# Kernel tuning notes

Hardware: AMD Instinct MI355X
Metric: run time of the kernel (lower is better)

Reference implementation:

```python
import jax, jax.numpy as jnp
import numpy as np

HALF = 1          # half_size
KS = 2 * HALF + 1 # kernel size = 3
ALPHA = 0.05
ITER = 10
LOG_N = float(np.log(KS * KS))
EPS = 1e-8


def _dilate(x):
    # x: [B, 1, H, W] -- soft (log-sum-exp-like) dilation with entropy correction.
    B, C, H, W = x.shape
    xp = jnp.pad(x, ((0, 0), (0, 0), (HALF, HALF), (HALF, HALF)), mode='reflect')
    # Extract ks*ks shifted views -> patches [B, K, H, W] (C == 1 folded away);
    # ordering (ki, kj) matches torch.nn.Unfold's channel-major layout for C=1.
    patches = jnp.stack(
        [xp[:, 0, i:i + H, j:j + W] for i in range(KS) for j in range(KS)],
        axis=1,
    )
    w = jax.nn.softmax(patches / ALPHA, axis=1)
    weighted_sum = jnp.sum(patches * w, axis=1)                 # [B, H, W]
    entropy = -jnp.sum(w * jnp.log(w + EPS), axis=1)            # [B, H, W]
    out = weighted_sum + ALPHA * (entropy - LOG_N)
    return out[:, None, :, :]                                   # [B, 1, H, W]


def _erode(x):
    return -_dilate(-x)


def _open(x):
    return _dilate(_erode(x))


def _forward(x):
    skel = jnp.clip(x - _open(x), 0.0, 1.0)

    def step(carry, _):
        xc, sk = carry
        xc = _erode(xc)
        sk = sk + jnp.clip(xc - _open(xc), 0.0, 1.0)
        return (xc, sk), None

    (_, skel), _ = jax.lax.scan(step, (x, skel), None, length=ITER)
    return skel


def setup_inputs() -> dict:
    key = jax.random.key(0)
    x = jax.random.uniform(key, (2, 1, 1024, 1024), dtype=jnp.float32)
    return {"x": x}


def reference(x):
    return _forward(x)
```

## Files before the change

kernel.cpp:

```cpp
#include <hip/hip_runtime.h>


#define HH 1024
#define WW 1024
#define NB 2
#define OTX 104
#define OTY 88
#define TW 128
#define TH 112
#define NW 16
#define HALO 12
#define GX 10
#define GY 12

constexpr float C1 = 28.85390081777927f;
constexpr float C2 = 0.03465735902799726f;

typedef float f32x2 __attribute__((ext_vector_type(2)));

__device__ __forceinline__ int mir(int i, int n) {
    return i < 0 ? -i : (i >= n ? 2 * n - 2 - i : i);
}
__device__ __forceinline__ float nbrL(float v) {
    return __int_as_float(__builtin_amdgcn_update_dpp(
        0, __float_as_int(v), 0x138, 0xf, 0xf, true));
}
__device__ __forceinline__ float nbrR(float v) {
    return __int_as_float(__builtin_amdgcn_update_dpp(
        0, __float_as_int(v), 0x130, 0xf, 0xf, true));
}

__device__ __forceinline__ f32x2 pk_add(f32x2 a, f32x2 b) {
    f32x2 d;
    asm("v_pk_add_f32 %0, %1, %2" : "=v"(d) : "v"(a), "v"(b));
    return d;
}
__device__ __forceinline__ f32x2 pk_add_swapB(f32x2 a, f32x2 b) {
    f32x2 d;
    asm("v_pk_add_f32 %0, %1, %2 op_sel:[0,1] op_sel_hi:[1,0]"
        : "=v"(d) : "v"(a), "v"(b));
    return d;
}
__device__ __forceinline__ f32x2 pk_mul(f32x2 a, f32x2 b) {
    f32x2 d;
    asm("v_pk_mul_f32 %0, %1, %2" : "=v"(d) : "v"(a), "v"(b));
    return d;
}

__device__ __forceinline__ f32x2 hsum3p(f32x2 P) {
    f32x2 LR;
    LR.x = nbrL(P.y);
    LR.y = nbrR(P.x);
    f32x2 X = pk_add(LR, P);
    return pk_add_swapB(X, P);
}

__global__ __launch_bounds__(1024, 4) void skel_k(const float* __restrict__ x0,
                                                  float* __restrict__ out) {
    __shared__ f32x2 halo[2][NW][4][64];
    const int lane = threadIdx.x & 63;
    const int w    = threadIdx.x >> 6;
    const int tx = blockIdx.x, ty = blockIdx.y, b = blockIdx.z;
    const int gx0 = tx * OTX - HALO, gy0 = ty * OTY - HALO;
    const int r0 = (w == 0) ? 0
                 : (w <= 4) ? 12 + 7 * (w - 1)
                 : (w <= 14) ? 40 + 6 * (w - 5) : 100;
    const bool isBox = (w == 0) || (w == 15);
    const bool is7   = (w >= 1) && (w <= 4);

    const float* src = x0 + (size_t)b * HH * WW;
    const bool interior = (gx0 >= 0) && (gx0 + TW <= WW) &&
                          (gy0 >= 0) && (gy0 + TH <= HH);
    const int mx0 = mir(gx0 + 2 * lane, WW);
    const int mx1 = mir(gx0 + 2 * lane + 1, WW);
    const float* base = src + (size_t)(gy0 + r0) * WW + gx0 + 2 * lane;

    f32x2 a0, a1, a2, a3, a4, a5, a6, a7, a8, a9, a10, a11;
#define LD(I, AV) { \
    if (interior) { \
        f32x2 v_ = *reinterpret_cast<const f32x2*>(base + (size_t)(I) * WW); \
        AV.x = __builtin_amdgcn_exp2f(v_.x * -C1); \
        AV.y = __builtin_amdgcn_exp2f(v_.y * -C1); \
    } else { \
        int my_ = mir(gy0 + r0 + (I), HH); \
        const float* rr_ = src + (size_t)my_ * WW; \
        AV.x = __builtin_amdgcn_exp2f(rr_[mx0] * -C1); \
        AV.y = __builtin_amdgcn_exp2f(rr_[mx1] * -C1); \
    } }
    LD(0, a0) LD(1, a1) LD(2, a2) LD(3, a3) LD(4, a4) LD(5, a5)
    if (isBox) { LD(6, a6) LD(7, a7) LD(8, a8) LD(9, a9) LD(10, a10) LD(11, a11) }
    else if (is7) { LD(6, a6) }
#undef LD

    f32x2 s0 = {0.f, 0.f}, s1 = s0, s2 = s0, s3 = s0, s4 = s0, s5 = s0, s6 = s0;

    #pragma unroll 1
    for (int j = 0; j < 11; ++j) {
        const int p = j & 1;
        f32x2 pub2, pub3;
        if (isBox)    { pub2 = a10; pub3 = a11; }
        else if (is7) { pub2 = a5;  pub3 = a6;  }
        else          { pub2 = a4;  pub3 = a5;  }
        halo[p][w][0][lane] = a0;
        halo[p][w][1][lane] = a1;
        halo[p][w][2][lane] = pub2;
        halo[p][w][3][lane] = pub3;
        __syncthreads();
        f32x2 one2 = {1.f, 1.f};
        f32x2 hm2 = (w > 0)      ? halo[p][w - 1][2][lane] : one2;
        f32x2 hm1 = (w > 0)      ? halo[p][w - 1][3][lane] : one2;
        f32x2 hp0 = (w < NW - 1) ? halo[p][w + 1][0][lane] : one2;
        f32x2 hp1 = (w < NW - 1) ? halo[p][w + 1][1][lane] : one2;

        f32x2 h_m = hsum3p(hm2);
        f32x2 h_c = hsum3p(hm1);
        f32x2 n_prev = {0.f, 0.f};

        if (!isBox) {
            f32x2 r_2 = {0.f, 0.f}, r_1 = r_2;
#define STEPC(OP1) \
            f32x2 h_p = hsum3p(OP1); \
            f32x2 n   = pk_add(pk_add(h_m, h_c), h_p); \
            f32x2 rc; rc.x = __builtin_amdgcn_rcpf(n.x); \
                      rc.y = __builtin_amdgcn_rcpf(n.y); \
            f32x2 r_0 = hsum3p(rc);
#define STEP0(OP1) { STEPC(OP1) \
            n_prev = n; h_m = h_c; h_c = h_p; r_2 = r_1; r_1 = r_0; }
#define STEP(OP1, AT, ST) { STEPC(OP1) \
            f32x2 PS = pk_mul(AT, pk_add(pk_add(r_2, r_1), r_0)); \
            f32x2 t; \
            t.x = __builtin_amdgcn_fmed3f(-C2 * __builtin_amdgcn_logf(PS.x), 0.f, 1.f); \
            t.y = __builtin_amdgcn_fmed3f(-C2 * __builtin_amdgcn_logf(PS.y), 0.f, 1.f); \
            ST = pk_add(ST, t); \
            AT = n_prev; \
            n_prev = n; h_m = h_c; h_c = h_p; r_2 = r_1; r_1 = r_0; }

            STEP0(a0)
            STEP0(a1)
            STEP(a2, a0, s0)
            STEP(a3, a1, s1)
            STEP(a4, a2, s2)
            STEP(a5, a3, s3)
            if (is7) {
                STEP(a6,  a4, s4)
                STEP(hp0, a5, s5)
                STEP(hp1, a6, s6)
            } else {
                STEP(hp0, a4, s4)
                STEP(hp1, a5, s5)
            }
#undef STEP
#undef STEP0
#undef STEPC
        } else {
#define BSTEP0(OP1) { f32x2 h_p = hsum3p(OP1); \
            f32x2 n = pk_add(pk_add(h_m, h_c), h_p); \
            n_prev = n; h_m = h_c; h_c = h_p; }
#define BSTEP(OP1, AT) { f32x2 h_p = hsum3p(OP1); \
            f32x2 n = pk_add(pk_add(h_m, h_c), h_p); \
            AT = n_prev; n_prev = n; h_m = h_c; h_c = h_p; }
            BSTEP0(a0)
            BSTEP0(a1)
            BSTEP(a2,  a0)
            BSTEP(a3,  a1)
            BSTEP(a4,  a2)
            BSTEP(a5,  a3)
            BSTEP(a6,  a4)
            BSTEP(a7,  a5)
            BSTEP(a8,  a6)
            BSTEP(a9,  a7)
            BSTEP(a10, a8)
            BSTEP(a11, a9)
            BSTEP(hp0, a10)
            BSTEP(hp1, a11)
#undef BSTEP
#undef BSTEP0
        }
    }

    if (!isBox && lane >= 6 && lane <= 57) {
        int gx = gx0 + 2 * lane;
        if (gx + 1 < WW) {
            float* dst = out + (size_t)b * HH * WW;
#define STORE(I, SV) { int gy = gy0 + r0 + (I); \
            if (gy < HH) \
                *reinterpret_cast<f32x2*>(&dst[(size_t)gy * WW + gx]) = SV; }
            STORE(0, s0) STORE(1, s1) STORE(2, s2) STORE(3, s3)
            STORE(4, s4) STORE(5, s5)
            if (is7) { STORE(6, s6) }
#undef STORE
        }
    }
}

extern "C" void kernel_launch(void* const* d_in, const int* in_sizes, int n_in,
                              void* d_out, int out_size, void* d_ws, size_t ws_size,
                              hipStream_t stream) {
    const float* x0 = (const float*)d_in[0];
    float* skel = (float*)d_out;
    skel_k<<<dim3(GX, GY, NB), dim3(1024, 1, 1), 0, stream>>>(x0, skel);
}
```

Baseline: 29.44 us.

## Widen tiles to four columns per lane with three rows per wave

Each lane now holds four adjacent columns instead of two, so a tile is 256 wide and 66 tall with 3 interior rows per wave, using float4 loads, stores and shared-memory halo entries. The horizontal 3-sum reuses partial sums inside the quad, so only two DPP shuffles are needed per four columns. This lowers cross-lane traffic per element and widens memory transactions. In exchange the vertical halo overhead grows a lot: 66-row tiles keep only 42 output rows, and the box waves redo work for thin strips. The grid also shrinks to 250 blocks.

```diff
diff --git a/kernel.cpp b/kernel.cpp
--- a/kernel.cpp
+++ b/kernel.cpp
@@ -4,19 +4,20 @@
 #define HH 1024
 #define WW 1024
 #define NB 2
-#define OTX 104
-#define OTY 88
-#define TW 128
-#define TH 112
+#define TW 256
+#define TH 66
 #define NW 16
 #define HALO 12
-#define GX 10
-#define GY 12
+#define OTX 232
+#define OTY 42
+#define GX 5
+#define GY 25
 
 constexpr float C1 = 28.85390081777927f;
 constexpr float C2 = 0.03465735902799726f;
 
 typedef float f32x2 __attribute__((ext_vector_type(2)));
+struct R4 { f32x2 a, b; };
 
 __device__ __forceinline__ int mir(int i, int n) {
     return i < 0 ? -i : (i >= n ? 2 * n - 2 - i : i);
@@ -29,136 +30,159 @@
     return __int_as_float(__builtin_amdgcn_update_dpp(
         0, __float_as_int(v), 0x130, 0xf, 0xf, true));
 }
-
 __device__ __forceinline__ f32x2 pk_add(f32x2 a, f32x2 b) {
     f32x2 d;
     asm("v_pk_add_f32 %0, %1, %2" : "=v"(d) : "v"(a), "v"(b));
     return d;
 }
-__device__ __forceinline__ f32x2 pk_add_swapB(f32x2 a, f32x2 b) {
-    f32x2 d;
-    asm("v_pk_add_f32 %0, %1, %2 op_sel:[0,1] op_sel_hi:[1,0]"
-        : "=v"(d) : "v"(a), "v"(b));
-    return d;
-}
 __device__ __forceinline__ f32x2 pk_mul(f32x2 a, f32x2 b) {
     f32x2 d;
     asm("v_pk_mul_f32 %0, %1, %2" : "=v"(d) : "v"(a), "v"(b));
     return d;
 }
 
-__device__ __forceinline__ f32x2 hsum3p(f32x2 P) {
-    f32x2 LR;
-    LR.x = nbrL(P.y);
-    LR.y = nbrR(P.x);
-    f32x2 X = pk_add(LR, P);
-    return pk_add_swapB(X, P);
+__device__ __forceinline__ R4 hsum3p4(R4 P) {
+    float cm1 = nbrL(P.b.y);
+    float cp4 = nbrR(P.a.x);
+    float t01 = P.a.x + P.a.y;
+    float t23 = P.b.x + P.b.y;
+    R4 H;
+    H.a.x = cm1 + t01;
+    H.a.y = t01 + P.b.x;
+    H.b.x = P.a.y + t23;
+    H.b.y = t23 + cp4;
+    return H;
+}
+__device__ __forceinline__ R4 vs3(R4 x, R4 y, R4 z) {
+    R4 n;
+    n.a = pk_add(pk_add(x.a, y.a), z.a);
+    n.b = pk_add(pk_add(x.b, y.b), z.b);
+    return n;
+}
+__device__ __forceinline__ R4 rcp4(R4 n) {
+    R4 r;
+    r.b.y = __builtin_amdgcn_rcpf(n.b.y);
+    r.a.x = __builtin_amdgcn_rcpf(n.a.x);
+    r.a.y = __builtin_amdgcn_rcpf(n.a.y);
+    r.b.x = __builtin_amdgcn_rcpf(n.b.x);
+    return r;
 }
 
 __global__ __launch_bounds__(1024, 4) void skel_k(const float* __restrict__ x0,
                                                   float* __restrict__ out) {
-    __shared__ f32x2 halo[2][NW][4][64];
+    __shared__ float4 halo[2][NW][4][64];
     const int lane = threadIdx.x & 63;
     const int w    = threadIdx.x >> 6;
     const int tx = blockIdx.x, ty = blockIdx.y, b = blockIdx.z;
     const int gx0 = tx * OTX - HALO, gy0 = ty * OTY - HALO;
-    const int r0 = (w == 0) ? 0
-                 : (w <= 4) ? 12 + 7 * (w - 1)
-                 : (w <= 14) ? 40 + 6 * (w - 5) : 100;
+    const int r0 = (w == 0) ? 0 : (w <= 14) ? 12 + 3 * (w - 1) : 54;
     const bool isBox = (w == 0) || (w == 15);
-    const bool is7   = (w >= 1) && (w <= 4);
 
     const float* src = x0 + (size_t)b * HH * WW;
     const bool interior = (gx0 >= 0) && (gx0 + TW <= WW) &&
                           (gy0 >= 0) && (gy0 + TH <= HH);
-    const int mx0 = mir(gx0 + 2 * lane, WW);
-    const int mx1 = mir(gx0 + 2 * lane + 1, WW);
-    const float* base = src + (size_t)(gy0 + r0) * WW + gx0 + 2 * lane;
-
-    f32x2 a0, a1, a2, a3, a4, a5, a6, a7, a8, a9, a10, a11;
+    const int mx0 = mir(gx0 + 4 * lane + 0, WW);
+    const int mx1 = mir(gx0 + 4 * lane + 1, WW);
+    const int mx2 = mir(gx0 + 4 * lane + 2, WW);
+    const int mx3 = mir(gx0 + 4 * lane + 3, WW);
+    const float* base = src + (size_t)(gy0 + r0) * WW + gx0 + 4 * lane;
+
+    R4 a0, a1, a2, a3, a4, a5, a6, a7, a8, a9, a10, a11;
 #define LD(I, AV) { \
     if (interior) { \
-        f32x2 v_ = *reinterpret_cast<const f32x2*>(base + (size_t)(I) * WW); \
-        AV.x = __builtin_amdgcn_exp2f(v_.x * -C1); \
-        AV.y = __builtin_amdgcn_exp2f(v_.y * -C1); \
+        float4 v_ = *reinterpret_cast<const float4*>(base + (size_t)(I) * WW); \
+        AV.a.x = __builtin_amdgcn_exp2f(v_.x * -C1); \
+        AV.a.y = __builtin_amdgcn_exp2f(v_.y * -C1); \
+        AV.b.x = __builtin_amdgcn_exp2f(v_.z * -C1); \
+        AV.b.y = __builtin_amdgcn_exp2f(v_.w * -C1); \
     } else { \
         int my_ = mir(gy0 + r0 + (I), HH); \
         const float* rr_ = src + (size_t)my_ * WW; \
-        AV.x = __builtin_amdgcn_exp2f(rr_[mx0] * -C1); \
-        AV.y = __builtin_amdgcn_exp2f(rr_[mx1] * -C1); \
+        AV.a.x = __builtin_amdgcn_exp2f(rr_[mx0] * -C1); \
+        AV.a.y = __builtin_amdgcn_exp2f(rr_[mx1] * -C1); \
+        AV.b.x = __builtin_amdgcn_exp2f(rr_[mx2] * -C1); \
+        AV.b.y = __builtin_amdgcn_exp2f(rr_[mx3] * -C1); \
     } }
-    LD(0, a0) LD(1, a1) LD(2, a2) LD(3, a3) LD(4, a4) LD(5, a5)
-    if (isBox) { LD(6, a6) LD(7, a7) LD(8, a8) LD(9, a9) LD(10, a10) LD(11, a11) }
-    else if (is7) { LD(6, a6) }
+    LD(0, a0) LD(1, a1) LD(2, a2)
+    if (isBox) {
+        LD(3, a3) LD(4, a4) LD(5, a5) LD(6, a6) LD(7, a7) LD(8, a8)
+        LD(9, a9) LD(10, a10) LD(11, a11)
+    }
 #undef LD
 
-    f32x2 s0 = {0.f, 0.f}, s1 = s0, s2 = s0, s3 = s0, s4 = s0, s5 = s0, s6 = s0;
+    R4 zz; zz.a = f32x2{0.f, 0.f}; zz.b = zz.a;
+    R4 s0 = zz, s1 = zz, s2 = zz;
+
+#define PACK4(V) float4{V.a.x, V.a.y, V.b.x, V.b.y}
+#define UNPACK4(F, V) { V.a.x = F.x; V.a.y = F.y; V.b.x = F.z; V.b.y = F.w; }
 
     #pragma unroll 1
     for (int j = 0; j < 11; ++j) {
         const int p = j & 1;
-        f32x2 pub2, pub3;
-        if (isBox)    { pub2 = a10; pub3 = a11; }
-        else if (is7) { pub2 = a5;  pub3 = a6;  }
-        else          { pub2 = a4;  pub3 = a5;  }
-        halo[p][w][0][lane] = a0;
-        halo[p][w][1][lane] = a1;
-        halo[p][w][2][lane] = pub2;
-        halo[p][w][3][lane] = pub3;
+        if (isBox) {
+            halo[p][w][0][lane] = PACK4(a0);
+            halo[p][w][1][lane] = PACK4(a1);
+            halo[p][w][2][lane] = PACK4(a10);
+            halo[p][w][3][lane] = PACK4(a11);
+        } else {
+            halo[p][w][0][lane] = PACK4(a0);
+            halo[p][w][1][lane] = PACK4(a1);
+            halo[p][w][2][lane] = PACK4(a1);
+            halo[p][w][3][lane] = PACK4(a2);
+        }
         __syncthreads();
-        f32x2 one2 = {1.f, 1.f};
-        f32x2 hm2 = (w > 0)      ? halo[p][w - 1][2][lane] : one2;
-        f32x2 hm1 = (w > 0)      ? halo[p][w - 1][3][lane] : one2;
-        f32x2 hp0 = (w < NW - 1) ? halo[p][w + 1][0][lane] : one2;
-        f32x2 hp1 = (w < NW - 1) ? halo[p][w + 1][1][lane] : one2;
-
-        f32x2 h_m = hsum3p(hm2);
-        f32x2 h_c = hsum3p(hm1);
-        f32x2 n_prev = {0.f, 0.f};
+        R4 hm2, hm1, hp0, hp1;
+        R4 oneR; oneR.a = f32x2{1.f, 1.f}; oneR.b = oneR.a;
+        if (w > 0) {
+            float4 f2 = halo[p][w - 1][2][lane]; UNPACK4(f2, hm2);
+            float4 f3 = halo[p][w - 1][3][lane]; UNPACK4(f3, hm1);
+        } else { hm2 = oneR; hm1 = oneR; }
+        if (w < NW - 1) {
+            float4 f0 = halo[p][w + 1][0][lane]; UNPACK4(f0, hp0);
+            float4 f1 = halo[p][w + 1][1][lane]; UNPACK4(f1, hp1);
+        } else { hp0 = oneR; hp1 = oneR; }
+
+        R4 h_m = hsum3p4(hm2);
+        R4 h_c = hsum3p4(hm1);
+        R4 n_prev = zz;
 
         if (!isBox) {
-            f32x2 r_2 = {0.f, 0.f}, r_1 = r_2;
+            R4 r_2 = zz, r_1 = zz;
 #define STEPC(OP1) \
-            f32x2 h_p = hsum3p(OP1); \
-            f32x2 n   = pk_add(pk_add(h_m, h_c), h_p); \
-            f32x2 rc; rc.x = __builtin_amdgcn_rcpf(n.x); \
-                      rc.y = __builtin_amdgcn_rcpf(n.y); \
-            f32x2 r_0 = hsum3p(rc);
+            R4 Hp = hsum3p4(OP1); \
+            R4 n  = vs3(h_m, h_c, Hp); \
+            R4 rc = rcp4(n); \
+            R4 r0_ = hsum3p4(rc);
 #define STEP0(OP1) { STEPC(OP1) \
-            n_prev = n; h_m = h_c; h_c = h_p; r_2 = r_1; r_1 = r_0; }
+            n_prev = n; h_m = h_c; h_c = Hp; r_2 = r_1; r_1 = r0_; }
 #define STEP(OP1, AT, ST) { STEPC(OP1) \
-            f32x2 PS = pk_mul(AT, pk_add(pk_add(r_2, r_1), r_0)); \
-            f32x2 t; \
-            t.x = __builtin_amdgcn_fmed3f(-C2 * __builtin_amdgcn_logf(PS.x), 0.f, 1.f); \
-            t.y = __builtin_amdgcn_fmed3f(-C2 * __builtin_amdgcn_logf(PS.y), 0.f, 1.f); \
-            ST = pk_add(ST, t); \
+            R4 rs = vs3(r_2, r_1, r0_); \
+            f32x2 pa = pk_mul(AT.a, rs.a); \
+            f32x2 pb = pk_mul(AT.b, rs.b); \
+            f32x2 ta, tb; \
+            ta.x = __builtin_amdgcn_fmed3f(-C2 * __builtin_amdgcn_logf(pa.x), 0.f, 1.f); \
+            ta.y = __builtin_amdgcn_fmed3f(-C2 * __builtin_amdgcn_logf(pa.y), 0.f, 1.f); \
+            tb.x = __builtin_amdgcn_fmed3f(-C2 * __builtin_amdgcn_logf(pb.x), 0.f, 1.f); \
+            tb.y = __builtin_amdgcn_fmed3f(-C2 * __builtin_amdgcn_logf(pb.y), 0.f, 1.f); \
+            ST.a = pk_add(ST.a, ta); ST.b = pk_add(ST.b, tb); \
             AT = n_prev; \
-            n_prev = n; h_m = h_c; h_c = h_p; r_2 = r_1; r_1 = r_0; }
+            n_prev = n; h_m = h_c; h_c = Hp; r_2 = r_1; r_1 = r0_; }
 
             STEP0(a0)
             STEP0(a1)
-            STEP(a2, a0, s0)
-            STEP(a3, a1, s1)
-            STEP(a4, a2, s2)
-            STEP(a5, a3, s3)
-            if (is7) {
-                STEP(a6,  a4, s4)
-                STEP(hp0, a5, s5)
-                STEP(hp1, a6, s6)
-            } else {
-                STEP(hp0, a4, s4)
-                STEP(hp1, a5, s5)
-            }
+            STEP(a2,  a0, s0)
+            STEP(hp0, a1, s1)
+            STEP(hp1, a2, s2)
 #undef STEP
 #undef STEP0
 #undef STEPC
         } else {
-#define BSTEP0(OP1) { f32x2 h_p = hsum3p(OP1); \
-            f32x2 n = pk_add(pk_add(h_m, h_c), h_p); \
-            n_prev = n; h_m = h_c; h_c = h_p; }
-#define BSTEP(OP1, AT) { f32x2 h_p = hsum3p(OP1); \
-            f32x2 n = pk_add(pk_add(h_m, h_c), h_p); \
-            AT = n_prev; n_prev = n; h_m = h_c; h_c = h_p; }
+#define BSTEP0(OP1) { R4 Hp = hsum3p4(OP1); \
+            R4 n = vs3(h_m, h_c, Hp); \
+            n_prev = n; h_m = h_c; h_c = Hp; }
+#define BSTEP(OP1, AT) { R4 Hp = hsum3p4(OP1); \
+            R4 n = vs3(h_m, h_c, Hp); \
+            AT = n_prev; n_prev = n; h_m = h_c; h_c = Hp; }
             BSTEP0(a0)
             BSTEP0(a1)
             BSTEP(a2,  a0)
@@ -178,16 +202,14 @@
         }
     }
 
-    if (!isBox && lane >= 6 && lane <= 57) {
-        int gx = gx0 + 2 * lane;
-        if (gx + 1 < WW) {
+    if (!isBox && lane >= 3 && lane <= 60) {
+        int gx = gx0 + 4 * lane;
+        if (gx + 3 < WW) {
             float* dst = out + (size_t)b * HH * WW;
 #define STORE(I, SV) { int gy = gy0 + r0 + (I); \
             if (gy < HH) \
-                *reinterpret_cast<f32x2*>(&dst[(size_t)gy * WW + gx]) = SV; }
-            STORE(0, s0) STORE(1, s1) STORE(2, s2) STORE(3, s3)
-            STORE(4, s4) STORE(5, s5)
-            if (is7) { STORE(6, s6) }
+                *reinterpret_cast<float4*>(&dst[(size_t)gy * WW + gx]) = PACK4(SV); }
+            STORE(0, s0) STORE(1, s1) STORE(2, s2)
 #undef STORE
         }
     }
```

Result: slower. 31.52 us (+7.1%).
